# Optimization experiments

Hardware: AMD Instinct MI355X
Metric: run time of the kernel (lower is better)

The kernel has to match this reference:

```python
import jax, jax.numpy as jnp
import numpy as np

N_COMPANY, N_INDUSTRY, E = 20000, 500, 8192
CC, CI, D, H = 256, 128, 256, 4


def setup_inputs() -> dict:
    key = jax.random.key(0)
    ks = jax.random.split(key, 14)
    p = lambda k, shape: (jax.random.normal(k, shape, jnp.float32) * 0.02)
    company_x = jax.random.normal(ks[0], (N_COMPANY, CC), jnp.float32)
    industry_x = jax.random.normal(ks[1], (N_INDUSTRY, CI), jnp.float32)
    src = jax.random.randint(ks[2], (E,), 0, N_COMPANY)
    tgt = jax.random.randint(ks[3], (E,), 0, N_INDUSTRY)
    edge_index = jnp.stack([src, tgt]).astype(jnp.int64)
    return {
        "company_x": company_x,
        "industry_x": industry_x,
        "edge_index": edge_index,
        "Wc": p(ks[4], (D, CC)), "bc": jnp.zeros((D,), jnp.float32),
        "Wi": p(ks[5], (D, CI)), "bi": jnp.zeros((D,), jnp.float32),
        "w_in": p(ks[6], (3 * D, D)), "b_in": jnp.zeros((3 * D,), jnp.float32),
        "w_out": p(ks[7], (D, D)), "b_out": jnp.zeros((D,), jnp.float32),
        "gamma": jnp.ones((D,), jnp.float32), "beta": jnp.zeros((D,), jnp.float32),
    }


def reference(company_x, industry_x, edge_index, Wc, bc, Wi, bi, w_in, b_in, w_out, b_out, gamma, beta):
    company_h = company_x @ Wc.T + bc          # [N, D]
    industry_h = industry_x @ Wi.T + bi        # [M, D]
    src, tgt = edge_index[0], edge_index[1]
    e = src.shape[0]
    d = company_h.shape[-1]
    hd = d // H

    q_in = company_h[src]                      # [E, D] gather
    kv_in = industry_h[tgt]                    # [E, D] gather

    wq, wk, wv = jnp.split(w_in, 3, axis=0)
    bq, bk, bv = jnp.split(b_in, 3)
    qh = (q_in @ wq.T + bq).reshape(e, H, hd)
    kh = (kv_in @ wk.T + bk).reshape(e, H, hd)
    vh = (kv_in @ wv.T + bv).reshape(e, H, hd)

    scale = 1.0 / jnp.sqrt(jnp.float32(hd))
    scores = jnp.einsum("qhd,khd->hqk", qh * scale, kh)   # [H, E, E]
    attn = jax.nn.softmax(scores, axis=-1)
    ctx = jnp.einsum("hqk,khd->qhd", attn, vh).reshape(e, d)
    attn_out = ctx @ w_out.T + b_out                        # [E, D]

    agg = jax.ops.segment_sum(attn_out, src, num_segments=company_h.shape[0])
    counts = jax.ops.segment_sum(jnp.ones((e,), jnp.float32), src, num_segments=company_h.shape[0])
    pooled = agg / (counts[:, None] + 1e-6)

    out = company_h + pooled
    mean = out.mean(-1, keepdims=True)
    var = out.var(-1, keepdims=True)
    return (out - mean) / jnp.sqrt(var + 1e-5) * gamma + beta
```

## Files before the change

### kernel.cpp

```cpp
#include <hip/hip_runtime.h>

#define E_EDGES 8192
#define N_COMP  20000
#define N_IND   500
#define NKEYS   512

typedef short bf16x8 __attribute__((ext_vector_type(8)));
typedef float f32x4  __attribute__((ext_vector_type(4)));

static __device__ __forceinline__ unsigned short f2bf(float v) {
    unsigned u = __builtin_bit_cast(unsigned, v);
    u = (u + 0x7FFFu + ((u >> 16) & 1u)) >> 16;
    return (unsigned short)u;
}

static __device__ __forceinline__ void cvt8(const float* __restrict__ s,
                                            unsigned short* __restrict__ d) {
    float4 a = *(const float4*)s;
    float4 b = *(const float4*)(s + 4);
    bf16x8 o;
    o[0] = (short)f2bf(a.x); o[1] = (short)f2bf(a.y);
    o[2] = (short)f2bf(a.z); o[3] = (short)f2bf(a.w);
    o[4] = (short)f2bf(b.x); o[5] = (short)f2bf(b.y);
    o[6] = (short)f2bf(b.z); o[7] = (short)f2bf(b.w);
    *(bf16x8*)d = o;
}

static __device__ __forceinline__ bf16x8 cvt8r(const float* __restrict__ s) {
    float4 a = *(const float4*)s;
    float4 b = *(const float4*)(s + 4);
    bf16x8 v;
    v[0] = (short)f2bf(a.x); v[1] = (short)f2bf(a.y);
    v[2] = (short)f2bf(a.z); v[3] = (short)f2bf(a.w);
    v[4] = (short)f2bf(b.x); v[5] = (short)f2bf(b.y);
    v[6] = (short)f2bf(b.z); v[7] = (short)f2bf(b.w);
    return v;
}

#define SWZ(r)   (((r) & 7) << 4)
#define SWZ4(r)  ((((r) >> 1) & 3) << 4)

static __device__ __forceinline__ void stage_f32(const float* src, char* base,
                                                 int sr, int sc) {
    *(bf16x8*)(base + ((sr * 64 + sc * 2) ^ SWZ(sr))) = cvt8r(src);
}

__global__ __launch_bounds__(256) void prep(
    const int* __restrict__ src, const int* __restrict__ tgt,
    const float* __restrict__ Wc, const float* __restrict__ Wi,
    const float* __restrict__ w_out, const float* __restrict__ w_in,
    const float* __restrict__ bc, const float* __restrict__ bi,
    const float* __restrict__ b_in,
    float* __restrict__ csrc, float* __restrict__ ctgt,
    unsigned short* __restrict__ Wc_bf, unsigned short* __restrict__ wout_bf,
    unsigned short* __restrict__ WcT_bf, unsigned short* __restrict__ Wi_bf,
    unsigned short* __restrict__ wkv_bf, float* __restrict__ beff)
{
    const int bid = blockIdx.x, tid = threadIdx.x;
    if (bid < 32) {
        int e = bid * 256 + tid;
        atomicAdd(&csrc[src[e]], 1.0f);
        atomicAdd(&ctgt[tgt[e]], 1.0f);
    } else if (bid < 64) {
        long i = ((long)(bid - 32) * 256 + tid) * 8;
        cvt8(Wc + i, Wc_bf + i);
    } else if (bid < 96) {
        long i = ((long)(bid - 64) * 256 + tid) * 8;
        cvt8(w_out + i, wout_bf + i);
    } else if (bid < 128) {
        long o = ((long)(bid - 96) * 256 + tid) * 8;
        int c = (int)(o >> 8), d0 = (int)(o & 255);
        bf16x8 v;
#pragma unroll
        for (int j = 0; j < 8; j++) v[j] = (short)f2bf(Wc[(long)(d0 + j) * 256 + c]);
        *(bf16x8*)(WcT_bf + o) = v;
    } else if (bid < 144) {
        long i = ((long)(bid - 128) * 256 + tid) * 8;
        cvt8(Wi + i, Wi_bf + i);
    } else if (bid < 208) {
        long i = ((long)(bid - 144) * 256 + tid) * 8;
        cvt8(w_in + 65536 + i, wkv_bf + i);
    } else {
        int gi = (bid - 208) * 256 + tid;
        int e = gi >> 2, q = gi & 3;
        const float* base = (e < 256) ? bc : bi;
        const float* wr = w_in + (long)e * 256 + q * 64;
        const float* br = base + q * 64;
        float s = 0.f;
#pragma unroll
        for (int j = 0; j < 64; j += 4) {
            float4 w4 = *(const float4*)(wr + j);
            float4 b4 = *(const float4*)(br + j);
            s += w4.x * b4.x + w4.y * b4.y + w4.z * b4.z + w4.w * b4.w;
        }
        s += __shfl_xor(s, 1);
        s += __shfl_xor(s, 2);
        if (q == 0) beff[e] = s + b_in[e];
    }
}

__global__ __launch_bounds__(256) void fusedW(
    const float* __restrict__ w_in, const unsigned short* __restrict__ WcT_bf,
    const float* __restrict__ industry_x, const unsigned short* __restrict__ Wi_bf,
    const unsigned short* __restrict__ wkv_bf, const float* __restrict__ beff,
    const float* __restrict__ ctgt, const float* __restrict__ csrc,
    unsigned short* __restrict__ Wcq_bf, unsigned short* __restrict__ Kbuf,
    unsigned short* __restrict__ VTg,
    float* __restrict__ cntT, int* __restrict__ list, int* __restrict__ nlist)
{
    const int bid = blockIdx.x;
    if (bid >= 20) {
        int i = (bid - 20) * 256 + threadIdx.x;
        if (i < NKEYS) cntT[(i & 15) * 32 + (i >> 4)] = ctgt[i];
        if (i < N_COMP && csrc[i] > 0.f) {
            int k = atomicAdd(nlist, 1);
            list[k] = i;
        }
        return;
    }

    __shared__ char lds[48 * 1024];
    const int t = threadIdx.x, wv = t >> 6, lane = t & 63;
    const int g = lane >> 4, ln = lane & 15;
    const int sr = t >> 2, sc = (t & 3) * 8;

    if (bid < 4) {
        char* ab = lds;
        char* wb = lds + 4 * 1024;
        const int bm = bid * 64;
        f32x4 acc[16];
#pragma unroll
        for (int i = 0; i < 16; i++) acc[i] = (f32x4){0.f, 0.f, 0.f, 0.f};
        const float* aptr = w_in + (long)(bm + sr) * 256 + sc;
        for (int kc = 0; kc < 256; kc += 32) {
            __syncthreads();
            stage_f32(aptr + kc, ab, sr, sc);
#pragma unroll
            for (int p = 0; p < 4; p++) {
                int r = p * 64 + sr;
                *(bf16x8*)(wb + ((r * 64 + sc * 2) ^ SWZ(r))) =
                    *(const bf16x8*)(WcT_bf + (long)r * 256 + kc + sc);
            }
            __syncthreads();
            int ar = wv * 16 + ln;
            bf16x8 af = *(bf16x8*)(ab + ((ar * 64 + g * 16) ^ SWZ(ar)));
#pragma unroll
            for (int nj = 0; nj < 16; nj++) {
                int wr = nj * 16 + ln;
                bf16x8 bf = *(bf16x8*)(wb + ((wr * 64 + g * 16) ^ SWZ(wr)));
                acc[nj] = __builtin_amdgcn_mfma_f32_16x16x32_bf16(af, bf, acc[nj], 0, 0, 0);
            }
        }
#pragma unroll
        for (int nj = 0; nj < 16; nj++)
#pragma unroll
            for (int r = 0; r < 4; r++)
                Wcq_bf[(long)(bm + wv * 16 + g * 4 + r) * 256 + nj * 16 + ln] =
                    f2bf(acc[nj][r]);
        return;
    }

    const int rg = (bid - 4) >> 1, colh = (bid - 4) & 1;
    char* ab  = lds;
    char* wb1 = lds + 4 * 1024;
    char* ihb = lds + 16 * 1024;
    char* wb2 = lds;

    {
        f32x4 a1[16];
#pragma unroll
        for (int i = 0; i < 16; i++) a1[i] = (f32x4){0.f, 0.f, 0.f, 0.f};
        int arow = rg * 64 + sr; if (arow > N_IND - 1) arow = N_IND - 1;
        const float* aptr = industry_x + (long)arow * 128 + sc;
        for (int kc = 0; kc < 128; kc += 32) {
            __syncthreads();
            stage_f32(aptr + kc, ab, sr, sc);
#pragma unroll
            for (int p = 0; p < 4; p++) {
                int r = p * 64 + sr;
                *(bf16x8*)(wb1 + ((r * 64 + sc * 2) ^ SWZ(r))) =
                    *(const bf16x8*)(Wi_bf + (long)r * 128 + kc + sc);
            }
            __syncthreads();
            int ar = wv * 16 + ln;
            bf16x8 af = *(bf16x8*)(ab + ((ar * 64 + g * 16) ^ SWZ(ar)));
#pragma unroll
            for (int nj = 0; nj < 16; nj++) {
                int wr = nj * 16 + ln;
                bf16x8 bf = *(bf16x8*)(wb1 + ((wr * 64 + g * 16) ^ SWZ(wr)));
                a1[nj] = __builtin_amdgcn_mfma_f32_16x16x32_bf16(af, bf, a1[nj], 0, 0, 0);
            }
        }
        __syncthreads();
#pragma unroll
        for (int nj = 0; nj < 16; nj++)
#pragma unroll
            for (int r = 0; r < 4; r++) {
                int row = wv * 16 + g * 4 + r, col = nj * 16 + ln;
                *(unsigned short*)(ihb + ((row * 512 + col * 2) ^ SWZ(row))) =
                    f2bf(a1[nj][r]);
            }
    }
    __syncthreads();

    if (colh == 0) {
        f32x4 a2[16];
#pragma unroll
        for (int i = 0; i < 16; i++) a2[i] = (f32x4){0.f, 0.f, 0.f, 0.f};
        for (int kc = 0; kc < 256; kc += 32) {
            __syncthreads();
#pragma unroll
            for (int p = 0; p < 4; p++) {
                int r = p * 64 + sr;
                *(bf16x8*)(wb2 + ((r * 64 + sc * 2) ^ SWZ(r))) =
                    *(const bf16x8*)(wkv_bf + (long)r * 256 + kc + sc);
            }
            __syncthreads();
            int row = wv * 16 + ln;
            bf16x8 af = *(bf16x8*)(ihb + ((row * 512 + (kc + g * 8) * 2) ^ SWZ(row)));
#pragma unroll
            for (int nj = 0; nj < 16; nj++) {
                int wr = nj * 16 + ln;
                bf16x8 bf = *(bf16x8*)(wb2 + ((wr * 64 + g * 16) ^ SWZ(wr)));
                a2[nj] = __builtin_amdgcn_mfma_f32_16x16x32_bf16(af, bf, a2[nj], 0, 0, 0);
            }
        }
#pragma unroll
        for (int nj = 0; nj < 16; nj++)
#pragma unroll
            for (int r = 0; r < 4; r++) {
                int R = rg * 64 + wv * 16 + g * 4 + r, n = nj * 16 + ln;
                Kbuf[(long)R * 256 + n] = f2bf(a2[nj][r] + beff[256 + n]);
            }
    } else {
        const unsigned short* wp = wkv_bf + 65536;
        f32x4 a2[16];
#pragma unroll
        for (int i = 0; i < 16; i++) a2[i] = (f32x4){0.f, 0.f, 0.f, 0.f};
        for (int kc = 0; kc < 256; kc += 32) {
            __syncthreads();
#pragma unroll
            for (int p = 0; p < 4; p++) {
                int r = p * 64 + sr;
                *(bf16x8*)(wb2 + ((r * 64 + sc * 2) ^ SWZ(r))) =
                    *(const bf16x8*)(wp + (long)r * 256 + kc + sc);
            }
            __syncthreads();
#pragma unroll
            for (int mi = 0; mi < 4; mi++) {
                int arow = wv * 64 + mi * 16 + ln;
                bf16x8 af = *(bf16x8*)(wb2 + ((arow * 64 + g * 16) ^ SWZ(arow)));
#pragma unroll
                for (int t4 = 0; t4 < 4; t4++) {
                    int brow = t4 * 16 + ln;
                    bf16x8 bfr = *(bf16x8*)(ihb + ((brow * 512 + (kc + g * 8) * 2) ^ SWZ(brow)));
                    a2[mi * 4 + t4] = __builtin_amdgcn_mfma_f32_16x16x32_bf16(af, bfr, a2[mi * 4 + t4], 0, 0, 0);
                }
            }
        }
#pragma unroll
        for (int mi = 0; mi < 4; mi++)
#pragma unroll
            for (int t4 = 0; t4 < 4; t4++)
#pragma unroll
                for (int r = 0; r < 4; r++) {
                    int nrow = wv * 64 + mi * 16 + g * 4 + r;
                    VTg[(long)nrow * 512 + rg * 64 + t4 * 16 + ln] =
                        f2bf(a2[mi * 4 + t4][r] + beff[512 + nrow]);
                }
    }
}

__global__ __launch_bounds__(256, 2) void megattn(
    const float* __restrict__ company_x,
    const unsigned short* __restrict__ Wcq,
    const float* __restrict__ beff,
    const unsigned short* __restrict__ Kbuf,
    const unsigned short* __restrict__ VTg,
    const float* __restrict__ cntT,
    const unsigned short* __restrict__ wout,
    const float* __restrict__ b_out,
    const int* __restrict__ list, const int* __restrict__ nlist,
    float* __restrict__ pooled)
{
    const int M = *nlist;
    const int bm = blockIdx.x * 16;
    if (bm >= M) return;

    __shared__ char lds[32768];
    const int t = threadIdx.x, h = t >> 6, lane = t & 63;
    const int g = lane >> 4, ln = lane & 15;
    char* qbase = lds + h * 2048;
    char* xbase = lds + 8192;
    char* pbase = lds + 16384 + h * 4096;

    {
        int row = t >> 4, c0 = (t & 15) * 16;
        int mr = bm + row; if (mr > M - 1) mr = M - 1;
        const float* src = company_x + (long)list[mr] * 256 + c0;
        *(bf16x8*)(xbase + ((row * 512 + c0 * 2) ^ SWZ(row))) = cvt8r(src);
        *(bf16x8*)(xbase + ((row * 512 + c0 * 2 + 16) ^ SWZ(row))) = cvt8r(src + 8);
    }
    __syncthreads();

    bf16x8 qf0, qf1;
    {
        f32x4 qa[4];
#pragma unroll
        for (int i = 0; i < 4; i++) qa[i] = (f32x4){0.f, 0.f, 0.f, 0.f};
#pragma unroll
        for (int kc = 0; kc < 256; kc += 32) {
            bf16x8 af = *(bf16x8*)(xbase + ((ln * 512 + (kc + g * 8) * 2) ^ SWZ(ln)));
#pragma unroll
            for (int nj = 0; nj < 4; nj++) {
                bf16x8 bf = *(const bf16x8*)(Wcq + (long)(h * 64 + nj * 16 + ln) * 256 + kc + g * 8);
                qa[nj] = __builtin_amdgcn_mfma_f32_16x16x32_bf16(af, bf, qa[nj], 0, 0, 0);
            }
        }
#pragma unroll
        for (int nj = 0; nj < 4; nj++)
#pragma unroll
            for (int r = 0; r < 4; r++) {
                int row = g * 4 + r, col = nj * 16 + ln;
                *(unsigned short*)(qbase + ((row * 128 + col * 2) ^ SWZ(row))) =
                    f2bf((qa[nj][r] + beff[h * 64 + col]) * 0.125f);
            }
        qf0 = *(bf16x8*)(qbase + ((ln * 128 + g * 16) ^ SWZ(ln)));
        qf1 = *(bf16x8*)(qbase + ((ln * 128 + 64 + g * 16) ^ SWZ(ln)));
    }

    f32x4 acc[4];
#pragma unroll
    for (int i = 0; i < 4; i++) acc[i] = (f32x4){0.f, 0.f, 0.f, 0.f};
    float mreg[4] = {-1e30f, -1e30f, -1e30f, -1e30f};
    float lreg[4] = {0.f, 0.f, 0.f, 0.f};

#pragma unroll
    for (int tile = 0; tile < 2; tile++) {
        float cnt[16];
        {
            const float* cp = cntT + ln * 32 + tile * 16;
#pragma unroll
            for (int j4 = 0; j4 < 4; j4++) {
                float4 c4 = *(const float4*)(cp + j4 * 4);
                cnt[j4 * 4 + 0] = c4.x; cnt[j4 * 4 + 1] = c4.y;
                cnt[j4 * 4 + 2] = c4.z; cnt[j4 * 4 + 3] = c4.w;
            }
        }

        f32x4 S[8][2];
#pragma unroll
        for (int half = 0; half < 2; half++) {
            bf16x8 k0r[4][2], k1r[4][2];
#pragma unroll
            for (int c4 = 0; c4 < 4; c4++)
#pragma unroll
                for (int sub = 0; sub < 2; sub++) {
                    const unsigned short* kr = Kbuf +
                        (long)(tile * 256 + (half * 4 + c4) * 32 + sub * 16 + ln) * 256 + h * 64 + g * 8;
                    k0r[c4][sub] = *(const bf16x8*)(kr);
                    k1r[c4][sub] = *(const bf16x8*)(kr + 32);
                }
#pragma unroll
            for (int c4 = 0; c4 < 4; c4++)
#pragma unroll
                for (int sub = 0; sub < 2; sub++) {
                    f32x4 s = (f32x4){0.f, 0.f, 0.f, 0.f};
                    s = __builtin_amdgcn_mfma_f32_16x16x32_bf16(qf0, k0r[c4][sub], s, 0, 0, 0);
                    s = __builtin_amdgcn_mfma_f32_16x16x32_bf16(qf1, k1r[c4][sub], s, 0, 0, 0);
                    S[half * 4 + c4][sub] = s;
                }
        }

        bf16x8 vr[2][2][4];
#pragma unroll
        for (int j = 0; j < 2; j++)
#pragma unroll
            for (int t4 = 0; t4 < 4; t4++)
                vr[0][j][t4] = *(const bf16x8*)(
                    VTg + (long)(h * 64 + t4 * 16 + ln) * 512 + tile * 256 + j * 32 + g * 8);

        float tm[4] = {-1e30f, -1e30f, -1e30f, -1e30f};
#pragma unroll
        for (int c = 0; c < 8; c++)
#pragma unroll
            for (int sub = 0; sub < 2; sub++)
#pragma unroll
                for (int r = 0; r < 4; r++) tm[r] = fmaxf(tm[r], S[c][sub][r]);
#pragma unroll
        for (int st = 1; st < 16; st <<= 1)
#pragma unroll
            for (int r = 0; r < 4; r++) tm[r] = fmaxf(tm[r], __shfl_xor(tm[r], st));

        float corr[4];
#pragma unroll
        for (int r = 0; r < 4; r++) {
            float mn = fmaxf(mreg[r], tm[r]);
            corr[r] = __expf(mreg[r] - mn);
            mreg[r] = mn;
        }

        float ps[4] = {0.f, 0.f, 0.f, 0.f};
#pragma unroll
        for (int c = 0; c < 8; c++)
#pragma unroll
            for (int sub = 0; sub < 2; sub++) {
                float cv = cnt[c * 2 + sub];
#pragma unroll
                for (int r = 0; r < 4; r++) {
                    float p = cv * __expf(S[c][sub][r] - mreg[r]);
                    S[c][sub][r] = p;
                    ps[r] += p;
                }
            }
#pragma unroll
        for (int st = 1; st < 16; st <<= 1)
#pragma unroll
            for (int r = 0; r < 4; r++) ps[r] += __shfl_xor(ps[r], st);
#pragma unroll
        for (int r = 0; r < 4; r++) lreg[r] = lreg[r] * corr[r] + ps[r];
#pragma unroll
        for (int i = 0; i < 4; i++)
#pragma unroll
            for (int r = 0; r < 4; r++) acc[i][r] *= corr[r];

#pragma unroll
        for (int grp = 0; grp < 4; grp++) {
            if (grp < 3) {
#pragma unroll
                for (int j = 0; j < 2; j++)
#pragma unroll
                    for (int t4 = 0; t4 < 4; t4++)
                        vr[(grp + 1) & 1][j][t4] = *(const bf16x8*)(
                            VTg + (long)(h * 64 + t4 * 16 + ln) * 512 +
                            tile * 256 + ((grp + 1) * 2 + j) * 32 + g * 8);
            }
#pragma unroll
            for (int j = 0; j < 2; j++) {
                int c = grp * 2 + j;
                char* pb = pbase + (c & 3) * 1024;
#pragma unroll
                for (int sub = 0; sub < 2; sub++)
#pragma unroll
                    for (int r = 0; r < 4; r++) {
                        int row = g * 4 + r;
                        *(unsigned short*)(pb + ((row * 64 + (sub * 16 + ln) * 2) ^ SWZ4(row))) =
                            f2bf(S[c][sub][r]);
                    }
                bf16x8 pa = *(bf16x8*)(pb + ((ln * 64 + g * 16) ^ SWZ4(ln)));
#pragma unroll
                for (int t4 = 0; t4 < 4; t4++)
                    acc[t4] = __builtin_amdgcn_mfma_f32_16x16x32_bf16(
                        pa, vr[grp & 1][j][t4], acc[t4], 0, 0, 0);
            }
        }
    }

#pragma unroll
    for (int t4 = 0; t4 < 4; t4++)
#pragma unroll
        for (int r = 0; r < 4; r++) {
            int row = g * 4 + r, col = t4 * 16 + ln;
            *(unsigned short*)(qbase + ((row * 128 + col * 2) ^ SWZ(row))) =
                f2bf(acc[t4][r] / lreg[r]);
        }
    __syncthreads();

    {
        f32x4 oa[4];
#pragma unroll
        for (int i = 0; i < 4; i++) oa[i] = (f32x4){0.f, 0.f, 0.f, 0.f};
#pragma unroll
        for (int kc = 0; kc < 256; kc += 32) {
            int hs = kc >> 6;
            int off = (kc & 63) + g * 8;
            bf16x8 af = *(bf16x8*)(lds + hs * 2048 + ((ln * 128 + off * 2) ^ SWZ(ln)));
#pragma unroll
            for (int nj = 0; nj < 4; nj++) {
                bf16x8 bf = *(const bf16x8*)(wout + (long)(h * 64 + nj * 16 + ln) * 256 + kc + g * 8);
                oa[nj] = __builtin_amdgcn_mfma_f32_16x16x32_bf16(af, bf, oa[nj], 0, 0, 0);
            }
        }
#pragma unroll
        for (int nj = 0; nj < 4; nj++) {
            int n = h * 64 + nj * 16 + ln;
            float bv = b_out[n];
#pragma unroll
            for (int r = 0; r < 4; r++) {
                int R = bm + g * 4 + r;
                if (R < M)
                    pooled[(long)list[R] * 256 + n] = oa[nj][r] + bv;
            }
        }
    }
}

__global__ __launch_bounds__(256) void gemm_ln(
    const float* __restrict__ A, const unsigned short* __restrict__ W,
    const float* __restrict__ bias,
    const float* __restrict__ pooled, const float* __restrict__ csrc,
    const float* __restrict__ gamma, const float* __restrict__ beta,
    float* __restrict__ out, int M, int K)
{
    __shared__ unsigned short As[64 * 32];
    __shared__ unsigned short Ws[256 * 32];
    char* abase = (char*)As;
    char* wbase = (char*)Ws;

    const int bm = blockIdx.x * 64;
    const int t = threadIdx.x;
    const int wv = t >> 6, lane = t & 63, g = lane >> 4, ln = lane & 15;

    f32x4 acc[16];
#pragma unroll
    for (int i = 0; i < 16; i++) acc[i] = (f32x4){0.f, 0.f, 0.f, 0.f};

    const int sr = t >> 2;
    const int sc = (t & 3) * 8;
    int arow = bm + sr; if (arow > M - 1) arow = M - 1;
    const float* aptr = A + (long)arow * K + sc;

    for (int kc = 0; kc < K; kc += 32) {
        __syncthreads();
        stage_f32(aptr + kc, abase, sr, sc);
#pragma unroll
        for (int p = 0; p < 4; p++) {
            int r = p * 64 + sr;
            *(bf16x8*)(wbase + ((r * 64 + sc * 2) ^ SWZ(r))) =
                *(const bf16x8*)(W + (long)r * K + kc + sc);
        }
        __syncthreads();

        const int ar = wv * 16 + ln;
        bf16x8 af = *(bf16x8*)(abase + ((ar * 64 + g * 16) ^ SWZ(ar)));
#pragma unroll
        for (int nj = 0; nj < 16; nj++) {
            int wr = nj * 16 + ln;
            bf16x8 bf = *(bf16x8*)(wbase + ((wr * 64 + g * 16) ^ SWZ(wr)));
            acc[nj] = __builtin_amdgcn_mfma_f32_16x16x32_bf16(af, bf, acc[nj], 0, 0, 0);
        }
    }

#pragma unroll
    for (int r = 0; r < 4; r++) {
        int R = bm + wv * 16 + g * 4 + r;
        bool valid = R < M;
        int Rc = valid ? R : 0;
        float cntv = csrc[Rc];
        float factor = (valid && cntv > 0.f) ? cntv / (cntv + 1e-6f) : 0.f;

        float v[16];
        float sum = 0.f, sq = 0.f;
#pragma unroll
        for (int nj = 0; nj < 16; nj++) {
            int n = nj * 16 + ln;
            float x = acc[nj][r] + bias[n] + factor * pooled[(long)Rc * 256 + n];
            v[nj] = x;
            sum += x;
            sq  += x * x;
        }
#pragma unroll
        for (int st = 1; st < 16; st <<= 1) {
            sum += __shfl_xor(sum, st);
            sq  += __shfl_xor(sq,  st);
        }
        float mean = sum * (1.0f / 256.0f);
        float var  = sq * (1.0f / 256.0f) - mean * mean;
        float rstd = rsqrtf(var + 1e-5f);
        if (valid) {
#pragma unroll
            for (int nj = 0; nj < 16; nj++) {
                int n = nj * 16 + ln;
                out[(long)R * 256 + n] = (v[nj] - mean) * rstd * gamma[n] + beta[n];
            }
        }
    }
}

extern "C" void kernel_launch(void* const* d_in, const int* in_sizes, int n_in,
                              void* d_out, int out_size, void* d_ws, size_t ws_size,
                              hipStream_t stream)
{
    const float* company_x  = (const float*)d_in[0];
    const float* industry_x = (const float*)d_in[1];
    const int*   edge       = (const int*)d_in[2];
    const float* Wc         = (const float*)d_in[3];
    const float* bc         = (const float*)d_in[4];
    const float* Wi         = (const float*)d_in[5];
    const float* bi         = (const float*)d_in[6];
    const float* w_in       = (const float*)d_in[7];
    const float* b_in       = (const float*)d_in[8];
    const float* w_out      = (const float*)d_in[9];
    const float* b_out      = (const float*)d_in[10];
    const float* gamma      = (const float*)d_in[11];
    const float* beta       = (const float*)d_in[12];
    float* out = (float*)d_out;

    const int* src = edge;
    const int* tgt = edge + E_EDGES;

    float* wf = (float*)d_ws;
    size_t o = 0;
    unsigned short* Wc_bf   = (unsigned short*)(wf + o); o += 32768;
    unsigned short* wout_bf = (unsigned short*)(wf + o); o += 32768;
    unsigned short* WcT_bf  = (unsigned short*)(wf + o); o += 32768;
    unsigned short* Wi_bf   = (unsigned short*)(wf + o); o += 16384;
    unsigned short* wkv_bf  = (unsigned short*)(wf + o); o += 65536;
    unsigned short* Wcq_bf  = (unsigned short*)(wf + o); o += 32768;
    unsigned short* Kbuf    = (unsigned short*)(wf + o); o += 65536;
    unsigned short* VTg     = (unsigned short*)(wf + o); o += 65536;
    float* pooled           = wf + o; o += (size_t)N_COMP * 256;
    float* beff             = wf + o; o += 768;
    float* cntT             = wf + o; o += NKEYS;
    int*   list             = (int*)(wf + o); o += E_EDGES;
    float* csrc             = wf + o; o += N_COMP;
    float* ctgt             = wf + o; o += NKEYS;
    int*   nlist            = (int*)(wf + o); o += 4;

    hipMemsetAsync(csrc, 0, (N_COMP + NKEYS + 4) * sizeof(float), stream);

    prep<<<dim3(220), dim3(256), 0, stream>>>(
        src, tgt, Wc, Wi, w_out, w_in, bc, bi, b_in,
        csrc, ctgt, Wc_bf, wout_bf, WcT_bf, Wi_bf, wkv_bf, beff);

    fusedW<<<dim3(99), dim3(256), 0, stream>>>(
        w_in, WcT_bf, industry_x, Wi_bf, wkv_bf, beff, ctgt, csrc,
        Wcq_bf, Kbuf, VTg, cntT, list, nlist);

    megattn<<<dim3(E_EDGES / 16), dim3(256), 0, stream>>>(
        company_x, Wcq_bf, beff, Kbuf, VTg, cntT, wout_bf, b_out,
        list, nlist, pooled);

    gemm_ln<<<dim3((N_COMP + 63) / 64), dim3(256), 0, stream>>>(
        company_x, Wc_bf, bc, pooled, csrc, gamma, beta, out, N_COMP, 256);
}
```

Baseline: 102.6 us.

## Merge prep and weight-fusion kernels, replace memset, build source list with atomic flags

Merges the weight-conversion prep kernel and the fused weight GEMM kernel into one launch. The separate memset is replaced by a zeroing block range, and the transposed/bf16 weight staging buffers are dropped in favor of converting raw fp32 weights on the fly inside the GEMM tiles. A new small kernel counts edges and builds the unique-source list through atomicCAS flags instead of scanning all companies, and megattn now reads target counts directly instead of through a transposed copy. This cuts launches and intermediate buffers, at the cost of redundant strided fp32 reads and conversions in the GEMM blocks, plus one extra tiny launch.

```diff
diff --git a/kernel.cpp b/kernel.cpp
--- a/kernel.cpp
+++ b/kernel.cpp
@@ -45,47 +45,51 @@
     *(bf16x8*)(base + ((sr * 64 + sc * 2) ^ SWZ(sr))) = cvt8r(src);
 }
 
-__global__ __launch_bounds__(256) void prep(
-    const int* __restrict__ src, const int* __restrict__ tgt,
+#define ZR_DWORDS (20000 + 512 + 4 + 20000)
+#define ZR_VEC4   ((ZR_DWORDS + 3) / 4)
+
+__global__ __launch_bounds__(256) void kernelA(
+    const float* __restrict__ industry_x,
     const float* __restrict__ Wc, const float* __restrict__ Wi,
     const float* __restrict__ w_out, const float* __restrict__ w_in,
     const float* __restrict__ bc, const float* __restrict__ bi,
     const float* __restrict__ b_in,
-    float* __restrict__ csrc, float* __restrict__ ctgt,
+    float* __restrict__ zregion,
     unsigned short* __restrict__ Wc_bf, unsigned short* __restrict__ wout_bf,
-    unsigned short* __restrict__ WcT_bf, unsigned short* __restrict__ Wi_bf,
-    unsigned short* __restrict__ wkv_bf, float* __restrict__ beff)
+    unsigned short* __restrict__ Wcq_bf, unsigned short* __restrict__ Kbuf,
+    unsigned short* __restrict__ VTg, float* __restrict__ beff)
 {
-    const int bid = blockIdx.x, tid = threadIdx.x;
-    if (bid < 32) {
-        int e = bid * 256 + tid;
-        atomicAdd(&csrc[src[e]], 1.0f);
-        atomicAdd(&ctgt[tgt[e]], 1.0f);
-    } else if (bid < 64) {
-        long i = ((long)(bid - 32) * 256 + tid) * 8;
+    __shared__ char lds[50176];
+    float* biasb = (float*)(lds + 49152);
+
+    const int bid = blockIdx.x, t = threadIdx.x;
+    const int wv = t >> 6, lane = t & 63;
+    const int g = lane >> 4, ln = lane & 15;
+    const int sr = t >> 2, sc = (t & 3) * 8;
+
+    if (bid < 40) {
+        int idx = bid * 256 + t;
+        if (idx < ZR_VEC4) {
+            float4 z = {0.f, 0.f, 0.f, 0.f};
+            *(float4*)(zregion + idx * 4) = z;
+        }
+        return;
+    }
+    if (bid < 72) {
+        long i = ((long)(bid - 40) * 256 + t) * 8;
         cvt8(Wc + i, Wc_bf + i);
-    } else if (bid < 96) {
-        long i = ((long)(bid - 64) * 256 + tid) * 8;
+        return;
+    }
+    if (bid < 104) {
+        long i = ((long)(bid - 72) * 256 + t) * 8;
         cvt8(w_out + i, wout_bf + i);
-    } else if (bid < 128) {
-        long o = ((long)(bid - 96) * 256 + tid) * 8;
-        int c = (int)(o >> 8), d0 = (int)(o & 255);
-        bf16x8 v;
-#pragma unroll
-        for (int j = 0; j < 8; j++) v[j] = (short)f2bf(Wc[(long)(d0 + j) * 256 + c]);
-        *(bf16x8*)(WcT_bf + o) = v;
-    } else if (bid < 144) {
-        long i = ((long)(bid - 128) * 256 + tid) * 8;
-        cvt8(Wi + i, Wi_bf + i);
-    } else if (bid < 208) {
-        long i = ((long)(bid - 144) * 256 + tid) * 8;
-        cvt8(w_in + 65536 + i, wkv_bf + i);
-    } else {
-        int gi = (bid - 208) * 256 + tid;
+        return;
+    }
+    if (bid < 108) {
+        int gi = (bid - 104) * 256 + t;
         int e = gi >> 2, q = gi & 3;
-        const float* base = (e < 256) ? bc : bi;
         const float* wr = w_in + (long)e * 256 + q * 64;
-        const float* br = base + q * 64;
+        const float* br = bc + q * 64;
         float s = 0.f;
 #pragma unroll
         for (int j = 0; j < 64; j += 4) {
@@ -96,38 +100,13 @@
         s += __shfl_xor(s, 1);
         s += __shfl_xor(s, 2);
         if (q == 0) beff[e] = s + b_in[e];
-    }
-}
-
-__global__ __launch_bounds__(256) void fusedW(
-    const float* __restrict__ w_in, const unsigned short* __restrict__ WcT_bf,
-    const float* __restrict__ industry_x, const unsigned short* __restrict__ Wi_bf,
-    const unsigned short* __restrict__ wkv_bf, const float* __restrict__ beff,
-    const float* __restrict__ ctgt, const float* __restrict__ csrc,
-    unsigned short* __restrict__ Wcq_bf, unsigned short* __restrict__ Kbuf,
-    unsigned short* __restrict__ VTg,
-    float* __restrict__ cntT, int* __restrict__ list, int* __restrict__ nlist)
-{
-    const int bid = blockIdx.x;
-    if (bid >= 20) {
-        int i = (bid - 20) * 256 + threadIdx.x;
-        if (i < NKEYS) cntT[(i & 15) * 32 + (i >> 4)] = ctgt[i];
-        if (i < N_COMP && csrc[i] > 0.f) {
-            int k = atomicAdd(nlist, 1);
-            list[k] = i;
-        }
         return;
     }
 
-    __shared__ char lds[48 * 1024];
-    const int t = threadIdx.x, wv = t >> 6, lane = t & 63;
-    const int g = lane >> 4, ln = lane & 15;
-    const int sr = t >> 2, sc = (t & 3) * 8;
-
-    if (bid < 4) {
+    if (bid < 112) {
         char* ab = lds;
         char* wb = lds + 4 * 1024;
-        const int bm = bid * 64;
+        const int bm = (bid - 108) * 64;
         f32x4 acc[16];
 #pragma unroll
         for (int i = 0; i < 16; i++) acc[i] = (f32x4){0.f, 0.f, 0.f, 0.f};
@@ -138,8 +117,11 @@
 #pragma unroll
             for (int p = 0; p < 4; p++) {
                 int r = p * 64 + sr;
-                *(bf16x8*)(wb + ((r * 64 + sc * 2) ^ SWZ(r))) =
-                    *(const bf16x8*)(WcT_bf + (long)r * 256 + kc + sc);
+                bf16x8 v;
+#pragma unroll
+                for (int j = 0; j < 8; j++)
+                    v[j] = (short)f2bf(Wc[(long)(kc + sc + j) * 256 + r]);
+                *(bf16x8*)(wb + ((r * 64 + sc * 2) ^ SWZ(r))) = v;
             }
             __syncthreads();
             int ar = wv * 16 + ln;
@@ -160,13 +142,26 @@
         return;
     }
 
-    const int rg = (bid - 4) >> 1, colh = (bid - 4) & 1;
+    const int rg = (bid - 112) >> 1, colh = (bid - 112) & 1;
     char* ab  = lds;
     char* wb1 = lds + 4 * 1024;
     char* ihb = lds + 16 * 1024;
     char* wb2 = lds;
 
     {
+        int e = 256 + colh * 256 + t;
+        const float* wr = w_in + (long)e * 256;
+        float s = 0.f;
+#pragma unroll
+        for (int j = 0; j < 256; j += 4) {
+            float4 w4 = *(const float4*)(wr + j);
+            float4 b4 = *(const float4*)(bi + j);
+            s += w4.x * b4.x + w4.y * b4.y + w4.z * b4.z + w4.w * b4.w;
+        }
+        biasb[t] = s + b_in[e];
+    }
+
+    {
         f32x4 a1[16];
 #pragma unroll
         for (int i = 0; i < 16; i++) a1[i] = (f32x4){0.f, 0.f, 0.f, 0.f};
@@ -179,7 +174,7 @@
             for (int p = 0; p < 4; p++) {
                 int r = p * 64 + sr;
                 *(bf16x8*)(wb1 + ((r * 64 + sc * 2) ^ SWZ(r))) =
-                    *(const bf16x8*)(Wi_bf + (long)r * 128 + kc + sc);
+                    cvt8r(Wi + (long)r * 128 + kc + sc);
             }
             __syncthreads();
             int ar = wv * 16 + ln;
@@ -203,6 +198,8 @@
     }
     __syncthreads();
 
+    const float* wraw = w_in + (long)(256 + colh * 256) * 256;
+
     if (colh == 0) {
         f32x4 a2[16];
 #pragma unroll
@@ -213,7 +210,7 @@
             for (int p = 0; p < 4; p++) {
                 int r = p * 64 + sr;
                 *(bf16x8*)(wb2 + ((r * 64 + sc * 2) ^ SWZ(r))) =
-                    *(const bf16x8*)(wkv_bf + (long)r * 256 + kc + sc);
+                    cvt8r(wraw + (long)r * 256 + kc + sc);
             }
             __syncthreads();
             int row = wv * 16 + ln;
@@ -230,10 +227,9 @@
 #pragma unroll
             for (int r = 0; r < 4; r++) {
                 int R = rg * 64 + wv * 16 + g * 4 + r, n = nj * 16 + ln;
-                Kbuf[(long)R * 256 + n] = f2bf(a2[nj][r] + beff[256 + n]);
+                Kbuf[(long)R * 256 + n] = f2bf(a2[nj][r] + biasb[n]);
             }
     } else {
-        const unsigned short* wp = wkv_bf + 65536;
         f32x4 a2[16];
 #pragma unroll
         for (int i = 0; i < 16; i++) a2[i] = (f32x4){0.f, 0.f, 0.f, 0.f};
@@ -243,7 +239,7 @@
             for (int p = 0; p < 4; p++) {
                 int r = p * 64 + sr;
                 *(bf16x8*)(wb2 + ((r * 64 + sc * 2) ^ SWZ(r))) =
-                    *(const bf16x8*)(wp + (long)r * 256 + kc + sc);
+                    cvt8r(wraw + (long)r * 256 + kc + sc);
             }
             __syncthreads();
 #pragma unroll
@@ -266,8 +262,23 @@
                 for (int r = 0; r < 4; r++) {
                     int nrow = wv * 64 + mi * 16 + g * 4 + r;
                     VTg[(long)nrow * 512 + rg * 64 + t4 * 16 + ln] =
-                        f2bf(a2[mi * 4 + t4][r] + beff[512 + nrow]);
+                        f2bf(a2[mi * 4 + t4][r] + biasb[nrow]);
                 }
+    }
+}
+
+__global__ __launch_bounds__(256) void kernelB(
+    const int* __restrict__ src, const int* __restrict__ tgt,
+    float* __restrict__ csrc, float* __restrict__ ctgt,
+    int* __restrict__ flags, int* __restrict__ nlist, int* __restrict__ list)
+{
+    int e = blockIdx.x * 256 + threadIdx.x;
+    int s = src[e];
+    atomicAdd(&csrc[s], 1.0f);
+    atomicAdd(&ctgt[tgt[e]], 1.0f);
+    if (atomicCAS(&flags[s], 0, 1) == 0) {
+        int k = atomicAdd(nlist, 1);
+        list[k] = s;
     }
 }
 
@@ -277,7 +288,7 @@
     const float* __restrict__ beff,
     const unsigned short* __restrict__ Kbuf,
     const unsigned short* __restrict__ VTg,
-    const float* __restrict__ cntT,
+    const float* __restrict__ ctgt,
     const unsigned short* __restrict__ wout,
     const float* __restrict__ b_out,
     const int* __restrict__ list, const int* __restrict__ nlist,
@@ -338,15 +349,9 @@
 #pragma unroll
     for (int tile = 0; tile < 2; tile++) {
         float cnt[16];
-        {
-            const float* cp = cntT + ln * 32 + tile * 16;
-#pragma unroll
-            for (int j4 = 0; j4 < 4; j4++) {
-                float4 c4 = *(const float4*)(cp + j4 * 4);
-                cnt[j4 * 4 + 0] = c4.x; cnt[j4 * 4 + 1] = c4.y;
-                cnt[j4 * 4 + 2] = c4.z; cnt[j4 * 4 + 3] = c4.w;
-            }
-        }
+#pragma unroll
+        for (int j = 0; j < 16; j++)
+            cnt[j] = ctgt[tile * 256 + (j >> 1) * 32 + (j & 1) * 16 + ln];
 
         f32x4 S[8][2];
 #pragma unroll
@@ -603,32 +608,27 @@
     size_t o = 0;
     unsigned short* Wc_bf   = (unsigned short*)(wf + o); o += 32768;
     unsigned short* wout_bf = (unsigned short*)(wf + o); o += 32768;
-    unsigned short* WcT_bf  = (unsigned short*)(wf + o); o += 32768;
-    unsigned short* Wi_bf   = (unsigned short*)(wf + o); o += 16384;
-    unsigned short* wkv_bf  = (unsigned short*)(wf + o); o += 65536;
     unsigned short* Wcq_bf  = (unsigned short*)(wf + o); o += 32768;
     unsigned short* Kbuf    = (unsigned short*)(wf + o); o += 65536;
     unsigned short* VTg     = (unsigned short*)(wf + o); o += 65536;
     float* pooled           = wf + o; o += (size_t)N_COMP * 256;
     float* beff             = wf + o; o += 768;
-    float* cntT             = wf + o; o += NKEYS;
     int*   list             = (int*)(wf + o); o += E_EDGES;
+    float* zregion          = wf + o;
     float* csrc             = wf + o; o += N_COMP;
     float* ctgt             = wf + o; o += NKEYS;
     int*   nlist            = (int*)(wf + o); o += 4;
-
-    hipMemsetAsync(csrc, 0, (N_COMP + NKEYS + 4) * sizeof(float), stream);
-
-    prep<<<dim3(220), dim3(256), 0, stream>>>(
-        src, tgt, Wc, Wi, w_out, w_in, bc, bi, b_in,
-        csrc, ctgt, Wc_bf, wout_bf, WcT_bf, Wi_bf, wkv_bf, beff);
-
-    fusedW<<<dim3(99), dim3(256), 0, stream>>>(
-        w_in, WcT_bf, industry_x, Wi_bf, wkv_bf, beff, ctgt, csrc,
-        Wcq_bf, Kbuf, VTg, cntT, list, nlist);
-
-    megattn<<<dim3(E_EDGES / 16), dim3(256), 0, stream>>>(
-        company_x, Wcq_bf, beff, Kbuf, VTg, cntT, wout_bf, b_out,
+    int*   flags            = (int*)(wf + o); o += N_COMP;
+
+    kernelA<<<dim3(128), dim3(256), 0, stream>>>(
+        industry_x, Wc, Wi, w_out, w_in, bc, bi, b_in,
+        zregion, Wc_bf, wout_bf, Wcq_bf, Kbuf, VTg, beff);
+
+    kernelB<<<dim3(E_EDGES / 256), dim3(256), 0, stream>>>(
+        src, tgt, csrc, ctgt, flags, nlist, list);
+
+    megattn<<<dim3(512), dim3(256), 0, stream>>>(
+        company_x, Wcq_bf, beff, Kbuf, VTg, ctgt, wout_bf, b_out,
         list, nlist, pooled);
 
     gemm_ln<<<dim3((N_COMP + 63) / 64), dim3(256), 0, stream>>>(
```

After: 106.3 us. 1.04x slower.

## Fold memset into prep kernel and move edge counting into fusedW

Applied to the files above, without the earlier changes.

Removes the hipMemsetAsync by zeroing the count/flag region inside the prep kernel. Edge counting and the build of the unique-source list move into the second kernel, which uses atomicCAS flags instead of scanning all companies. The cntT transpose buffer is dropped and megattn reads ctgt with a strided index. The aim is fewer launches and less serial work before attention, at the cost of more atomics and uncoalesced count loads.

```diff
diff --git a/kernel.cpp b/kernel.cpp
--- a/kernel.cpp
+++ b/kernel.cpp
@@ -45,43 +45,47 @@
     *(bf16x8*)(base + ((sr * 64 + sc * 2) ^ SWZ(sr))) = cvt8r(src);
 }
 
-__global__ __launch_bounds__(256) void prep(
-    const int* __restrict__ src, const int* __restrict__ tgt,
+#define ZR_DWORDS (20000 + 512 + 4 + 20000)
+#define ZR_VEC4   ((ZR_DWORDS + 3) / 4)
+
+__global__ __launch_bounds__(256) void prepZ(
     const float* __restrict__ Wc, const float* __restrict__ Wi,
     const float* __restrict__ w_out, const float* __restrict__ w_in,
     const float* __restrict__ bc, const float* __restrict__ bi,
     const float* __restrict__ b_in,
-    float* __restrict__ csrc, float* __restrict__ ctgt,
+    float* __restrict__ zregion,
     unsigned short* __restrict__ Wc_bf, unsigned short* __restrict__ wout_bf,
     unsigned short* __restrict__ WcT_bf, unsigned short* __restrict__ Wi_bf,
     unsigned short* __restrict__ wkv_bf, float* __restrict__ beff)
 {
     const int bid = blockIdx.x, tid = threadIdx.x;
-    if (bid < 32) {
-        int e = bid * 256 + tid;
-        atomicAdd(&csrc[src[e]], 1.0f);
-        atomicAdd(&ctgt[tgt[e]], 1.0f);
-    } else if (bid < 64) {
-        long i = ((long)(bid - 32) * 256 + tid) * 8;
+    if (bid < 40) {
+        int idx = bid * 256 + tid;
+        if (idx < ZR_VEC4) {
+            float4 z = {0.f, 0.f, 0.f, 0.f};
+            *(float4*)(zregion + idx * 4) = z;
+        }
+    } else if (bid < 72) {
+        long i = ((long)(bid - 40) * 256 + tid) * 8;
         cvt8(Wc + i, Wc_bf + i);
-    } else if (bid < 96) {
-        long i = ((long)(bid - 64) * 256 + tid) * 8;
+    } else if (bid < 104) {
+        long i = ((long)(bid - 72) * 256 + tid) * 8;
         cvt8(w_out + i, wout_bf + i);
-    } else if (bid < 128) {
-        long o = ((long)(bid - 96) * 256 + tid) * 8;
+    } else if (bid < 136) {
+        long o = ((long)(bid - 104) * 256 + tid) * 8;
         int c = (int)(o >> 8), d0 = (int)(o & 255);
         bf16x8 v;
 #pragma unroll
         for (int j = 0; j < 8; j++) v[j] = (short)f2bf(Wc[(long)(d0 + j) * 256 + c]);
         *(bf16x8*)(WcT_bf + o) = v;
-    } else if (bid < 144) {
-        long i = ((long)(bid - 128) * 256 + tid) * 8;
+    } else if (bid < 152) {
+        long i = ((long)(bid - 136) * 256 + tid) * 8;
         cvt8(Wi + i, Wi_bf + i);
-    } else if (bid < 208) {
-        long i = ((long)(bid - 144) * 256 + tid) * 8;
+    } else if (bid < 216) {
+        long i = ((long)(bid - 152) * 256 + tid) * 8;
         cvt8(w_in + 65536 + i, wkv_bf + i);
     } else {
-        int gi = (bid - 208) * 256 + tid;
+        int gi = (bid - 216) * 256 + tid;
         int e = gi >> 2, q = gi & 3;
         const float* base = (e < 256) ? bc : bi;
         const float* wr = w_in + (long)e * 256 + q * 64;
@@ -99,22 +103,25 @@
     }
 }
 
-__global__ __launch_bounds__(256) void fusedW(
+__global__ __launch_bounds__(256) void fusedWB(
     const float* __restrict__ w_in, const unsigned short* __restrict__ WcT_bf,
     const float* __restrict__ industry_x, const unsigned short* __restrict__ Wi_bf,
     const unsigned short* __restrict__ wkv_bf, const float* __restrict__ beff,
-    const float* __restrict__ ctgt, const float* __restrict__ csrc,
+    const int* __restrict__ src, const int* __restrict__ tgt,
+    float* __restrict__ csrc, float* __restrict__ ctgt,
+    int* __restrict__ flags, int* __restrict__ nlist, int* __restrict__ list,
     unsigned short* __restrict__ Wcq_bf, unsigned short* __restrict__ Kbuf,
-    unsigned short* __restrict__ VTg,
-    float* __restrict__ cntT, int* __restrict__ list, int* __restrict__ nlist)
+    unsigned short* __restrict__ VTg)
 {
     const int bid = blockIdx.x;
     if (bid >= 20) {
-        int i = (bid - 20) * 256 + threadIdx.x;
-        if (i < NKEYS) cntT[(i & 15) * 32 + (i >> 4)] = ctgt[i];
-        if (i < N_COMP && csrc[i] > 0.f) {
+        int e = (bid - 20) * 256 + threadIdx.x;
+        int s = src[e];
+        atomicAdd(&csrc[s], 1.0f);
+        atomicAdd(&ctgt[tgt[e]], 1.0f);
+        if (atomicCAS(&flags[s], 0, 1) == 0) {
             int k = atomicAdd(nlist, 1);
-            list[k] = i;
+            list[k] = s;
         }
         return;
     }
@@ -277,7 +284,7 @@
     const float* __restrict__ beff,
     const unsigned short* __restrict__ Kbuf,
     const unsigned short* __restrict__ VTg,
-    const float* __restrict__ cntT,
+    const float* __restrict__ ctgt,
     const unsigned short* __restrict__ wout,
     const float* __restrict__ b_out,
     const int* __restrict__ list, const int* __restrict__ nlist,
@@ -338,15 +345,9 @@
 #pragma unroll
     for (int tile = 0; tile < 2; tile++) {
         float cnt[16];
-        {
-            const float* cp = cntT + ln * 32 + tile * 16;
-#pragma unroll
-            for (int j4 = 0; j4 < 4; j4++) {
-                float4 c4 = *(const float4*)(cp + j4 * 4);
-                cnt[j4 * 4 + 0] = c4.x; cnt[j4 * 4 + 1] = c4.y;
-                cnt[j4 * 4 + 2] = c4.z; cnt[j4 * 4 + 3] = c4.w;
-            }
-        }
+#pragma unroll
+        for (int j = 0; j < 16; j++)
+            cnt[j] = ctgt[tile * 256 + (j >> 1) * 32 + (j & 1) * 16 + ln];
 
         f32x4 S[8][2];
 #pragma unroll
@@ -611,24 +612,24 @@
     unsigned short* VTg     = (unsigned short*)(wf + o); o += 65536;
     float* pooled           = wf + o; o += (size_t)N_COMP * 256;
     float* beff             = wf + o; o += 768;
-    float* cntT             = wf + o; o += NKEYS;
     int*   list             = (int*)(wf + o); o += E_EDGES;
+    float* zregion          = wf + o;
     float* csrc             = wf + o; o += N_COMP;
     float* ctgt             = wf + o; o += NKEYS;
     int*   nlist            = (int*)(wf + o); o += 4;
-
-    hipMemsetAsync(csrc, 0, (N_COMP + NKEYS + 4) * sizeof(float), stream);
-
-    prep<<<dim3(220), dim3(256), 0, stream>>>(
-        src, tgt, Wc, Wi, w_out, w_in, bc, bi, b_in,
-        csrc, ctgt, Wc_bf, wout_bf, WcT_bf, Wi_bf, wkv_bf, beff);
-
-    fusedW<<<dim3(99), dim3(256), 0, stream>>>(
-        w_in, WcT_bf, industry_x, Wi_bf, wkv_bf, beff, ctgt, csrc,
-        Wcq_bf, Kbuf, VTg, cntT, list, nlist);
-
-    megattn<<<dim3(E_EDGES / 16), dim3(256), 0, stream>>>(
-        company_x, Wcq_bf, beff, Kbuf, VTg, cntT, wout_bf, b_out,
+    int*   flags            = (int*)(wf + o); o += N_COMP;
+
+    prepZ<<<dim3(228), dim3(256), 0, stream>>>(
+        Wc, Wi, w_out, w_in, bc, bi, b_in,
+        zregion, Wc_bf, wout_bf, WcT_bf, Wi_bf, wkv_bf, beff);
+
+    fusedWB<<<dim3(52), dim3(256), 0, stream>>>(
+        w_in, WcT_bf, industry_x, Wi_bf, wkv_bf, beff,
+        src, tgt, csrc, ctgt, flags, nlist, list,
+        Wcq_bf, Kbuf, VTg);
+
+    megattn<<<dim3(512), dim3(256), 0, stream>>>(
+        company_x, Wcq_bf, beff, Kbuf, VTg, ctgt, wout_bf, b_out,
         list, nlist, pooled);
 
     gemm_ln<<<dim3((N_COMP + 63) / 64), dim3(256), 0, stream>>>(
```

After: 95.92 us. 6.5% less time.
